# Optimization experiments

Measured on AMD Instinct MI355X. Metric: run time of the kernel, lower is better.

## Reference

```python
import jax, jax.numpy as jnp
import numpy as np

ITEM_NUM = 100000
EMBED = 128
HIDDEN = 256
BETA = 0.5
B = 4096
H = 200

def setup_inputs() -> dict:
    key = jax.random.key(0)
    ks = jax.random.split(key, 7)
    history = jax.random.randint(ks[0], (B, H), 0, ITEM_NUM)
    target = jax.random.randint(ks[1], (B,), 0, ITEM_NUM)
    embed_history = jax.random.normal(ks[2], (ITEM_NUM, EMBED), dtype=jnp.float32) * 0.01
    embed_target = jax.random.normal(ks[3], (ITEM_NUM, EMBED), dtype=jnp.float32) * 0.01
    # nn.Linear default init: U(-1/sqrt(fan_in), 1/sqrt(fan_in)); biases zeroed by _init_weight_
    lim1 = 1.0 / np.sqrt(EMBED)
    W1 = jax.random.uniform(ks[4], (EMBED, HIDDEN), dtype=jnp.float32, minval=-lim1, maxval=lim1)
    b1 = jnp.zeros((HIDDEN,), dtype=jnp.float32)
    lim2 = 1.0 / np.sqrt(HIDDEN)
    w2 = jax.random.uniform(ks[5], (HIDDEN,), dtype=jnp.float32, minval=-lim2, maxval=lim2)
    return {"history": history, "target": target, "embed_history": embed_history,
            "embed_target": embed_target, "W1": W1, "b1": b1, "w2": w2}

def reference(history, target, embed_history, embed_target, W1, b1, w2):
    hist_e = embed_history[history]            # [B, H, d]
    tgt_e = embed_target[target][:, None, :]   # [B, 1, d]
    x = hist_e * tgt_e                          # [B, H, d]
    a = jnp.einsum('bhk,k->bh', jax.nn.relu(jnp.einsum('bhd,dk->bhk', x, W1) + b1), w2)  # [B, H]
    mask = (history != target[:, None]).astype(a.dtype)  # [B, H]
    exp_A = jnp.exp(a) * mask                  # [B, H]
    denom = jnp.sum(exp_A, axis=-1) ** BETA    # [B], beta-power normalization (not softmax)
    attn = exp_A / denom[:, None]              # [B, H]
    pred = jnp.einsum('bh,bhd,bd->b', attn, hist_e, tgt_e[:, 0, :])  # [B]
    return jax.nn.sigmoid(pred)
```

## Files before the change

### kernel.cpp

```cpp
#include <hip/hip_runtime.h>

#define B_SZ   4096
#define H_SZ   200
#define D_SZ   128
#define N_SZ   256
#define ROWS   (B_SZ * H_SZ)
#define BM     64
#define TPB    8
#define RPB    (BM * TPB)
#define NBLK   (ROWS / RPB)

typedef _Float16 f16;
typedef __attribute__((ext_vector_type(2))) _Float16 f16x2;
typedef __attribute__((ext_vector_type(8))) _Float16 f16x8;
typedef __attribute__((ext_vector_type(4))) float f32x4;

union H8 { f16x8 v; f16x2 p[4]; uint4 u; };

__device__ __forceinline__ f16x2 pkrtz(float a, float b) {
    return __builtin_bit_cast(f16x2, __builtin_amdgcn_cvt_pkrtz(a, b));
}

__global__ __launch_bounds__(256) void cvt_eh(const float* __restrict__ src,
                                              uint4* __restrict__ dst, int n8) {
    int i = blockIdx.x * 256 + threadIdx.x;
    if (i >= n8) return;
    const f32x4* p = (const f32x4*)src + (size_t)i * 2;
    f32x4 a = p[0], b = p[1];
    uint4 o;
    o.x = __builtin_bit_cast(unsigned, pkrtz(a[0], a[1]));
    o.y = __builtin_bit_cast(unsigned, pkrtz(a[2], a[3]));
    o.z = __builtin_bit_cast(unsigned, pkrtz(b[0], b[1]));
    o.w = __builtin_bit_cast(unsigned, pkrtz(b[2], b[3]));
    dst[i] = o;
}

__global__ __launch_bounds__(256) void cvt_w1(const float* __restrict__ src,
                                              f16* __restrict__ dst) {
    int i = blockIdx.x * 256 + threadIdx.x;
    int n = i >> 7, d = i & 127;
    dst[i] = (f16)(src[d * N_SZ + n] * 0.0625f);
}

__global__ __launch_bounds__(256) void zero_acc(float* __restrict__ s1g,
                                                float* __restrict__ s2g) {
    int i = blockIdx.x * 256 + threadIdx.x;
    if (i < B_SZ) { s1g[i] = 0.f; s2g[i] = 0.f; }
}

__global__ __launch_bounds__(512, 4) void nais_main(
    const int* __restrict__ history, const int* __restrict__ target,
    const uint4* __restrict__ ehh, const float* __restrict__ et,
    const f16* __restrict__ w1t, const float* __restrict__ b1,
    const float* __restrict__ w2,
    float* __restrict__ s1g, float* __restrict__ s2g)
{
    __shared__ uint4 AbufV[2][BM * 256 / 16];
    __shared__ float apart[2][8][BM];
    __shared__ f16   tgt_h[4][D_SZ];
    __shared__ int   tgt_i[4];
    __shared__ float dotd_lds[3][BM];
    __shared__ float m_lds[3][BM];

    const int tid  = threadIdx.x;
    const int wid  = tid >> 6;
    const int lane = tid & 63;
    const int lo   = lane & 15;
    const int hi   = lane >> 4;
    const int row  = tid >> 3;
    const int seg  = tid & 7;
    const int blk  = blockIdx.x;
    const int b_base = (blk * RPB) / H_SZ;

    if (tid < 4) {
        int bb = b_base + tid;
        tgt_i[tid] = target[bb < B_SZ ? bb : (B_SZ - 1)];
    }
    __syncthreads();
    if (tid < 256) {
        const int r4 = tid >> 6, j = (tid & 63) * 2;
        const float* src = et + (size_t)tgt_i[r4] * D_SZ + j;
        ((f16x2*)tgt_h)[tid] = pkrtz(src[0] * 16.f, src[1] * 16.f);
    }

    f16x8 wfrag[4][2];
    #pragma unroll
    for (int ni = 0; ni < 2; ++ni) {
        int n = 32 * wid + 16 * ni + lo;
        #pragma unroll
        for (int ki = 0; ki < 4; ++ki)
            wfrag[ki][ni] = *(const f16x8*)(w1t + (size_t)n * D_SZ + 32 * ki + 8 * hi);
    }
    const int n0 = 32 * wid + 4 * hi;
    const f32x4 b1a = *(const f32x4*)(b1 + n0);
    const f32x4 b1b = *(const f32x4*)(b1 + n0 + 16);
    const f32x4 w2a = *(const f32x4*)(w2 + n0);
    const f32x4 w2b = *(const f32x4*)(w2 + n0 + 16);

    const int grow0 = blk * RPB + row;
    const int* hrow = history + grow0;
    int ih_cur = hrow[0];
    int ih_nxt = hrow[BM];
    uint4 hq0, hq1;
    {
        const uint4* p = ehh + (size_t)ih_cur * 16;
        hq0 = p[seg]; hq1 = p[8 + seg];
    }
    int b_loc = grow0 / H_SZ - b_base;
    int rem   = grow0 - (b_loc + b_base) * H_SZ;
    __syncthreads();

    #define REDUCE(TT)                                                            \
    {                                                                             \
        const float* ap = &apart[(TT) & 1][0][tid];                               \
        float a = ap[0];                                                          \
        _Pragma("unroll")                                                         \
        for (int w = 1; w < 8; ++w) a += ap[w * BM];                              \
        const int slot = (TT) % 3;                                                \
        float e   = m_lds[slot][tid] * __expf(a);                                 \
        float s2t = e * dotd_lds[slot][tid];                                      \
        const int b = (blk * RPB + (TT) * BM + tid) / H_SZ;                       \
        const int blo = __shfl(b, 0);                                             \
        const bool ishi = (b != blo);                                             \
        float e_lo = ishi ? 0.f : e,  d_lo = ishi ? 0.f : s2t;                    \
        float e_hi = ishi ? e : 0.f,  d_hi = ishi ? s2t : 0.f;                    \
        _Pragma("unroll")                                                         \
        for (int o = 1; o < 64; o <<= 1) {                                        \
            e_lo += __shfl_xor(e_lo, o); d_lo += __shfl_xor(d_lo, o);             \
            e_hi += __shfl_xor(e_hi, o); d_hi += __shfl_xor(d_hi, o);             \
        }                                                                         \
        if (tid == 0)          { atomicAdd(&s1g[blo], e_lo); atomicAdd(&s2g[blo], d_lo); } \
        if (tid == 63 && ishi) { atomicAdd(&s1g[b],   e_hi); atomicAdd(&s2g[b],   d_hi); } \
    }

    for (int t = 0; t < TPB; ++t) {
        char* Ab = (char*)AbufV[t & 1];

        {
            H8 h1, h2, t1, t2, x1, x2;
            h1.u = hq0; h2.u = hq1;
            t1.v = *(const f16x8*)&tgt_h[b_loc][8 * seg];
            t2.v = *(const f16x8*)&tgt_h[b_loc][64 + 8 * seg];
            x1.v = h1.v * t1.v;
            x2.v = h2.v * t2.v;
            float s = 0.f;
            #pragma unroll
            for (int j = 0; j < 4; ++j) {
                s = __builtin_amdgcn_fdot2(h1.p[j], t1.p[j], s, false);
                s = __builtin_amdgcn_fdot2(h2.p[j], t2.p[j], s, false);
            }
            s += __shfl_xor(s, 1);
            s += __shfl_xor(s, 2);
            s += __shfl_xor(s, 4);
            if (seg == 0) {
                dotd_lds[t % 3][row] = s;
                m_lds[t % 3][row] = (ih_cur != tgt_i[b_loc]) ? 1.f : 0.f;
            }
            const unsigned sw = (unsigned)((row & 7) << 4);
            char* rb = Ab + row * 256;
            *(uint4*)(rb + (((unsigned)(16 * seg)) ^ sw))          = x1.u;
            *(uint4*)(rb + (128u + (((unsigned)(16 * seg)) ^ sw))) = x2.u;
        }
        __syncthreads();

        if (t + 1 < TPB) {
            ih_cur = ih_nxt;
            if (t + 2 < TPB) ih_nxt = hrow[(t + 2) * BM];
            const uint4* p = ehh + (size_t)ih_cur * 16;
            hq0 = p[seg]; hq1 = p[8 + seg];
        }

        if (t > 0 && tid < BM) REDUCE(t - 1)

        #pragma unroll
        for (int mi = 0; mi < 4; ++mi) {
            const int rr = 16 * mi + lo;
            const unsigned swr = (unsigned)((rr & 7) << 4);
            f16x8 af[4];
            #pragma unroll
            for (int ki = 0; ki < 4; ++ki) {
                unsigned off = ((unsigned)(64 * ki + 16 * hi)) ^ swr;
                af[ki] = *(const f16x8*)(Ab + rr * 256 + off);
            }
            f32x4 acc0 = b1a;
            f32x4 acc1 = b1b;
            __builtin_amdgcn_s_setprio(1);
            #pragma unroll
            for (int ki = 0; ki < 4; ++ki) {
                acc0 = __builtin_amdgcn_mfma_f32_16x16x32_f16(wfrag[ki][0], af[ki], acc0, 0, 0, 0);
                acc1 = __builtin_amdgcn_mfma_f32_16x16x32_f16(wfrag[ki][1], af[ki], acc1, 0, 0, 0);
            }
            __builtin_amdgcn_s_setprio(0);
            float v = fmaxf(acc0[0], 0.f) * w2a[0] + fmaxf(acc1[0], 0.f) * w2b[0];
            v += fmaxf(acc0[1], 0.f) * w2a[1] + fmaxf(acc1[1], 0.f) * w2b[1];
            v += fmaxf(acc0[2], 0.f) * w2a[2] + fmaxf(acc1[2], 0.f) * w2b[2];
            v += fmaxf(acc0[3], 0.f) * w2a[3] + fmaxf(acc1[3], 0.f) * w2b[3];
            v += __shfl_xor(v, 16);
            v += __shfl_xor(v, 32);
            if (lane < 16) apart[t & 1][wid][16 * mi + lane] = v;
        }

        rem += BM;
        if (rem >= H_SZ) { rem -= H_SZ; ++b_loc; }
    }
    __syncthreads();
    if (tid < BM) REDUCE(TPB - 1)
    #undef REDUCE
}

__global__ __launch_bounds__(256) void nais_sig(const float* __restrict__ s1g,
                                                const float* __restrict__ s2g,
                                                float* __restrict__ out) {
    int b = blockIdx.x * 256 + threadIdx.x;
    if (b >= B_SZ) return;
    float pred = 0.0625f * s2g[b] / sqrtf(s1g[b]);
    out[b] = 1.f / (1.f + __expf(-pred));
}

extern "C" void kernel_launch(void* const* d_in, const int* in_sizes, int n_in,
                              void* d_out, int out_size, void* d_ws, size_t ws_size,
                              hipStream_t stream) {
    const int*   history = (const int*)d_in[0];
    const int*   target  = (const int*)d_in[1];
    const float* eh      = (const float*)d_in[2];
    const float* et      = (const float*)d_in[3];
    const float* W1      = (const float*)d_in[4];
    const float* b1      = (const float*)d_in[5];
    const float* w2      = (const float*)d_in[6];
    float* out = (float*)d_out;

    char* ws = (char*)d_ws;
    uint4* ehh = (uint4*)ws;
    f16*   w1t = (f16*)(ws + (size_t)100000 * D_SZ * 2);
    float* s1g = (float*)(ws + (size_t)100000 * D_SZ * 2 + N_SZ * D_SZ * 2);
    float* s2g = s1g + B_SZ;

    const int n8 = 100000 * D_SZ / 8;
    cvt_eh<<<(n8 + 255) / 256, 256, 0, stream>>>(eh, ehh, n8);
    cvt_w1<<<(N_SZ * D_SZ) / 256, 256, 0, stream>>>(W1, w1t);
    zero_acc<<<(B_SZ + 255) / 256, 256, 0, stream>>>(s1g, s2g);
    nais_main<<<NBLK, 512, 0, stream>>>(history, target, ehh, et, w1t, b1, w2, s1g, s2g);
    nais_sig<<<(B_SZ + 255) / 256, 256, 0, stream>>>(s1g, s2g, out);
}
```

Baseline: 105.0 us.

## Parallelize per-tile reduction across all threads and accumulate per-block in LDS

The per-tile attention reduction used to run on one wavefront, with serial sums over 8 partials and 6-step butterfly shuffles. It now runs on all 512 threads: each thread reads one partial, a 3-step xor shuffle combines the 8 segments, and results go through LDS atomics into per-block 4-entry accumulators. Those are flushed once to global memory at the end, which cuts global atomics. The weight conversion and accumulator-zeroing kernels are merged into one launch, and the apart array is padded to 72 to avoid bank conflicts. LDS atomic contention within a row-group and an extra final barrier are the added costs.

Result: no change. 106.9 us (+1.8%).

```diff
diff --git a/kernel.cpp b/kernel.cpp
--- a/kernel.cpp
+++ b/kernel.cpp
@@ -35,17 +35,17 @@
     dst[i] = o;
 }
 
-__global__ __launch_bounds__(256) void cvt_w1(const float* __restrict__ src,
-                                              f16* __restrict__ dst) {
+__global__ __launch_bounds__(256) void cvt_w1z(const float* __restrict__ src,
+                                               f16* __restrict__ dst,
+                                               float* __restrict__ s1g,
+                                               float* __restrict__ s2g) {
     int i = blockIdx.x * 256 + threadIdx.x;
-    int n = i >> 7, d = i & 127;
-    dst[i] = (f16)(src[d * N_SZ + n] * 0.0625f);
-}
-
-__global__ __launch_bounds__(256) void zero_acc(float* __restrict__ s1g,
-                                                float* __restrict__ s2g) {
-    int i = blockIdx.x * 256 + threadIdx.x;
-    if (i < B_SZ) { s1g[i] = 0.f; s2g[i] = 0.f; }
+    if (i < N_SZ * D_SZ) {
+        int n = i >> 7, d = i & 127;
+        dst[i] = (f16)(src[d * N_SZ + n] * 0.0625f);
+    }
+    int z = i - N_SZ * D_SZ;
+    if (z >= 0 && z < B_SZ) { s1g[z] = 0.f; s2g[z] = 0.f; }
 }
 
 __global__ __launch_bounds__(512, 4) void nais_main(
@@ -56,11 +56,12 @@
     float* __restrict__ s1g, float* __restrict__ s2g)
 {
     __shared__ uint4 AbufV[2][BM * 256 / 16];
-    __shared__ float apart[2][8][BM];
+    __shared__ float apart[2][8][72];
     __shared__ f16   tgt_h[4][D_SZ];
     __shared__ int   tgt_i[4];
     __shared__ float dotd_lds[3][BM];
     __shared__ float m_lds[3][BM];
+    __shared__ float s1_loc[4], s2_loc[4];
 
     const int tid  = threadIdx.x;
     const int wid  = tid >> 6;
@@ -75,6 +76,7 @@
     if (tid < 4) {
         int bb = b_base + tid;
         tgt_i[tid] = target[bb < B_SZ ? bb : (B_SZ - 1)];
+        s1_loc[tid] = 0.f; s2_loc[tid] = 0.f;
     }
     __syncthreads();
     if (tid < 256) {
@@ -108,29 +110,22 @@
     }
     int b_loc = grow0 / H_SZ - b_base;
     int rem   = grow0 - (b_loc + b_base) * H_SZ;
-    __syncthreads();
-
-    #define REDUCE(TT)                                                            \
+    int b_prev = b_loc;
+    __syncthreads();
+
+    #define REDUCE(TT, PAR)                                                       \
     {                                                                             \
-        const float* ap = &apart[(TT) & 1][0][tid];                               \
-        float a = ap[0];                                                          \
-        _Pragma("unroll")                                                         \
-        for (int w = 1; w < 8; ++w) a += ap[w * BM];                              \
-        const int slot = (TT) % 3;                                                \
-        float e   = m_lds[slot][tid] * __expf(a);                                 \
-        float s2t = e * dotd_lds[slot][tid];                                      \
-        const int b = (blk * RPB + (TT) * BM + tid) / H_SZ;                       \
-        const int blo = __shfl(b, 0);                                             \
-        const bool ishi = (b != blo);                                             \
-        float e_lo = ishi ? 0.f : e,  d_lo = ishi ? 0.f : s2t;                    \
-        float e_hi = ishi ? e : 0.f,  d_hi = ishi ? s2t : 0.f;                    \
-        _Pragma("unroll")                                                         \
-        for (int o = 1; o < 64; o <<= 1) {                                        \
-            e_lo += __shfl_xor(e_lo, o); d_lo += __shfl_xor(d_lo, o);             \
-            e_hi += __shfl_xor(e_hi, o); d_hi += __shfl_xor(d_hi, o);             \
+        float av = apart[PAR][seg][row];                                          \
+        av += __shfl_xor(av, 1);                                                  \
+        av += __shfl_xor(av, 2);                                                  \
+        av += __shfl_xor(av, 4);                                                  \
+        if (seg == 0) {                                                           \
+            const int slot = (TT) % 3;                                            \
+            float e   = m_lds[slot][row] * __expf(av);                            \
+            float s2t = e * dotd_lds[slot][row];                                  \
+            atomicAdd(&s1_loc[b_prev], e);                                        \
+            atomicAdd(&s2_loc[b_prev], s2t);                                      \
         }                                                                         \
-        if (tid == 0)          { atomicAdd(&s1g[blo], e_lo); atomicAdd(&s2g[blo], d_lo); } \
-        if (tid == 63 && ishi) { atomicAdd(&s1g[b],   e_hi); atomicAdd(&s2g[b],   d_hi); } \
     }
 
     for (int t = 0; t < TPB; ++t) {
@@ -170,7 +165,7 @@
             hq0 = p[seg]; hq1 = p[8 + seg];
         }
 
-        if (t > 0 && tid < BM) REDUCE(t - 1)
+        if (t > 0) REDUCE(t - 1, (t - 1) & 1)
 
         #pragma unroll
         for (int mi = 0; mi < 4; ++mi) {
@@ -200,12 +195,18 @@
             if (lane < 16) apart[t & 1][wid][16 * mi + lane] = v;
         }
 
+        b_prev = b_loc;
         rem += BM;
         if (rem >= H_SZ) { rem -= H_SZ; ++b_loc; }
     }
     __syncthreads();
-    if (tid < BM) REDUCE(TPB - 1)
+    REDUCE(TPB - 1, (TPB - 1) & 1)
     #undef REDUCE
+    __syncthreads();
+    if (tid < 4 && b_base + tid < B_SZ) {
+        atomicAdd(&s1g[b_base + tid], s1_loc[tid]);
+        atomicAdd(&s2g[b_base + tid], s2_loc[tid]);
+    }
 }
 
 __global__ __launch_bounds__(256) void nais_sig(const float* __restrict__ s1g,
@@ -237,8 +238,7 @@
 
     const int n8 = 100000 * D_SZ / 8;
     cvt_eh<<<(n8 + 255) / 256, 256, 0, stream>>>(eh, ehh, n8);
-    cvt_w1<<<(N_SZ * D_SZ) / 256, 256, 0, stream>>>(W1, w1t);
-    zero_acc<<<(B_SZ + 255) / 256, 256, 0, stream>>>(s1g, s2g);
+    cvt_w1z<<<(N_SZ * D_SZ + B_SZ + 255) / 256, 256, 0, stream>>>(W1, w1t, s1g, s2g);
     nais_main<<<NBLK, 512, 0, stream>>>(history, target, ehh, et, w1t, b1, w2, s1g, s2g);
     nais_sig<<<(B_SZ + 255) / 256, 256, 0, stream>>>(s1g, s2g, out);
 }
```
